# Kernel optimization log

Measured on AMD Instinct MI355X. Metric: run time of the kernel, lower is better.

## Reference

```python
import math
import jax, jax.numpy as jnp
import numpy as np

B, H, W = 2, 128, 128
HW = H * W
D, NH, NL, KS = 256, 8, 1, 5
NP = KS * KS
HD = D // NH
DFF = 1024
KEEP = 0.25
H_SIZE = 188.0
EPS = 1e-5


def _layernorm(x, g, b):
    m = x.mean(-1, keepdims=True)
    v = ((x - m) ** 2).mean(-1, keepdims=True)
    return (x - m) * jax.lax.rsqrt(v + EPS) * g + b


def _mha(q_in, k_in, v_in, w_qkv, b_qkv, w_o, b_o):
    wq, wk, wv = jnp.split(w_qkv, 3, axis=0)
    bq, bk, bv = jnp.split(b_qkv, 3, axis=0)
    def heads(x, w, b):
        y = x @ w.T + b
        return y.reshape(y.shape[0], y.shape[1], NH, HD)
    q, k, v = heads(q_in, wq, bq), heads(k_in, wk, bk), heads(v_in, wv, bv)
    scores = jnp.einsum('bqhd,bkhd->bhqk', q, k) / math.sqrt(HD)
    attn = jax.nn.softmax(scores, axis=-1)
    out = jnp.einsum('bhqk,bkhd->bqhd', attn, v).reshape(q_in.shape[0], q_in.shape[1], D)
    return out @ w_o.T + b_o


def _bilinear(v, grid):
    # v: (B, HW, NH, HD); grid: (B, LQ, NH, NP, 2) normalized (x, y) in [0,1]
    x = grid[..., 0] * W - 0.5
    y = grid[..., 1] * H - 0.5
    x0 = jnp.floor(x); y0 = jnp.floor(y)
    lx = x - x0; ly = y - y0
    x0i = x0.astype(jnp.int32); y0i = y0.astype(jnp.int32)
    bidx = jnp.arange(v.shape[0])[:, None, None, None]
    hidx = jnp.arange(NH)[None, None, :, None]
    def corner(xi, yi, wgt):
        valid = (xi >= 0) & (xi < W) & (yi >= 0) & (yi < H)  # zero-pad outside
        idx = jnp.clip(yi, 0, H - 1) * W + jnp.clip(xi, 0, W - 1)
        s = v[bidx, idx, hidx]  # (B, LQ, NH, NP, HD)
        return s * (wgt * valid)[..., None]
    return (corner(x0i, y0i, (1 - lx) * (1 - ly))
            + corner(x0i + 1, y0i, lx * (1 - ly))
            + corner(x0i, y0i + 1, (1 - lx) * ly)
            + corner(x0i + 1, y0i + 1, lx * ly))


def _where_to_attend(query, ref_windows, lbw, lbb, sow, sob, kernel_indices):
    Bq, L = ref_windows.shape[:2]
    ob = (query @ lbw.T + lbb).reshape(Bq, L, NH, NL, 4)  # with_rotation=False -> 4 vars
    rw = ref_windows[:, :, None, None, :]  # (B, L, 1, 1, 7)
    ref_boxes = rw[..., jnp.array([0, 1, 3, 4])]
    ref_angles = rw[..., 6:7]
    angles = jnp.broadcast_to(ref_angles, (Bq, L, NH, NL, 1))
    boxes = ref_boxes + ob / 8.0 * ref_boxes[..., jnp.array([2, 3, 2, 3])]
    center = boxes[..., None, :2]  # (B, L, NH, NL, 1, 2)
    size = boxes[..., None, 2:]
    cos_a, sin_a = jnp.cos(angles), jnp.sin(angles)
    rot = jnp.stack([cos_a, -sin_a, sin_a, cos_a], -1).reshape(Bq, L, NH, NL, 1, 2, 2)
    dgrid = (query @ sow.T + sob).reshape(Bq, L, NH, NL, NP, 2) / H_SIZE
    fg = kernel_indices * jax.nn.relu(size)              # (B, L, NH, NL, NP, 2)
    fg = center + (fg[..., None, :] * rot).sum(-1)       # rotate then shift
    return fg + dgrid


def _box_attn(query, value, ref_windows, vpw, vpb, law, lab, lbw, lbb, sow, sob, ow, ob_, kernel_indices):
    Bq, LQ = query.shape[:2]
    LV = value.shape[1]
    v = (value @ vpw.T + vpb).reshape(Bq, LV, NH, HD)
    aw = jax.nn.softmax((query @ law.T + lab).reshape(Bq, LQ, NH, NL * NP), axis=-1)
    aw = aw.reshape(Bq, LQ, NH, NL, NP)
    grid = _where_to_attend(query, ref_windows, lbw, lbb, sow, sob, kernel_indices)
    sampled = _bilinear(v, grid[:, :, :, 0])             # single level (NL=1)
    out = (aw[:, :, :, 0, :, None] * sampled).sum(-2).reshape(Bq, LQ, D)
    return out @ ow.T + ob_


def _forward(src, pos, ref_windows, score_mask, in_proj_w, in_proj_b, mha_out_w, mha_out_b,
             value_proj_w, value_proj_b, linear_attn_w, linear_attn_b, linear_box_w, linear_box_b,
             samp_off_w, samp_off_b, ca_out_w, ca_out_b, lin1_w, lin1_b, lin2_w, lin2_b,
             qn_g, qn_b, n1_g, n1_b, n2_g, n2_b, kernel_indices):
    Bq = src.shape[0]
    fg_num = math.ceil(src.shape[1] * KEEP)
    sel_score, indices = jax.lax.top_k(score_mask, fg_num)
    gather = lambda x, i: jnp.take_along_axis(x, i[..., None], axis=1)
    sel_src = gather(src, indices)
    sel_pos = gather(pos, indices)
    sel_ref = gather(ref_windows, indices)
    q_num = math.ceil(fg_num * KEEP)
    q_idx = jax.lax.top_k(sel_score, q_num)[1]
    q_src = gather(sel_src, q_idx)
    q_pos = gather(sel_pos, q_idx)
    qk = q_src + q_pos
    q2 = _mha(qk, qk, q_src, in_proj_w, in_proj_b, mha_out_w, mha_out_b)
    q_src = _layernorm(q_src + q2, qn_g, qn_b)
    brow = jnp.arange(Bq)[:, None]
    sel_src = sel_src.at[brow, q_idx].set(q_src)
    src2 = _box_attn(sel_src + sel_pos, src, sel_ref, value_proj_w, value_proj_b,
                     linear_attn_w, linear_attn_b, linear_box_w, linear_box_b,
                     samp_off_w, samp_off_b, ca_out_w, ca_out_b, kernel_indices)
    sel_src = _layernorm(sel_src + src2, n1_g, n1_b)
    ff = jax.nn.relu(sel_src @ lin1_w.T + lin1_b) @ lin2_w.T + lin2_b
    sel_src = _layernorm(sel_src + ff, n2_g, n2_b)
    return src.at[brow, indices].set(sel_src)


def setup_inputs() -> dict:
    key = jax.random.key(0)
    ks = jax.random.split(key, 16)
    def w(k, shape):
        return jax.random.normal(k, shape, dtype=jnp.float32) * 0.02
    # deformable sampling-offsets bias init (per-head directional grid)
    thetas = np.arange(NH) * (2.0 * np.pi / NH)
    g = np.stack([np.cos(thetas), np.sin(thetas)], -1)
    g = g / np.abs(g).max(-1, keepdims=True)
    g = np.tile(g.reshape(NH, 1, 1, 2), (1, NL, NP, 1)) * (np.arange(NP) + 1).reshape(1, 1, NP, 1)
    samp_off_b = jnp.asarray(g.reshape(-1), dtype=jnp.float32)
    # fixed kernel indices buffer (odd kernel, (x,y) order, /kernel_size)
    ind = np.linspace(-(KS - 1) / 2, (KS - 1) / 2, KS)
    ii, jj = np.meshgrid(ind, ind, indexing='ij')
    kernel_indices = jnp.asarray(np.stack([jj, ii], -1).reshape(-1, 2) / KS, dtype=jnp.float32)
    return dict(
        src=jax.random.normal(ks[0], (B, HW, D), dtype=jnp.float32),
        pos=jax.random.normal(ks[1], (B, HW, D), dtype=jnp.float32),
        src_shape=jnp.array([[H, W]], dtype=jnp.int32),
        src_start_idx=jnp.zeros((1,), dtype=jnp.int32),
        ref_windows=jax.random.uniform(ks[2], (B, HW, 7), dtype=jnp.float32),
        score_mask=jax.random.normal(ks[3], (B, HW), dtype=jnp.float32),
        in_proj_w=w(ks[4], (3 * D, D)), in_proj_b=jnp.zeros((3 * D,), jnp.float32),
        mha_out_w=w(ks[5], (D, D)), mha_out_b=jnp.zeros((D,), jnp.float32),
        value_proj_w=w(ks[6], (D, D)), value_proj_b=jnp.zeros((D,), jnp.float32),
        linear_attn_w=w(ks[7], (NH * NL * NP, D)), linear_attn_b=jnp.zeros((NH * NL * NP,), jnp.float32),
        linear_box_w=w(ks[8], (NL * NH * 4, D)), linear_box_b=jnp.zeros((NL * NH * 4,), jnp.float32),
        samp_off_w=w(ks[9], (NH * NL * NP * 2, D)), samp_off_b=samp_off_b,
        ca_out_w=w(ks[10], (D, D)), ca_out_b=jnp.zeros((D,), jnp.float32),
        lin1_w=w(ks[11], (DFF, D)), lin1_b=jnp.zeros((DFF,), jnp.float32),
        lin2_w=w(ks[12], (D, DFF)), lin2_b=jnp.zeros((D,), jnp.float32),
        qn_g=jnp.ones((D,), jnp.float32), qn_b=jnp.zeros((D,), jnp.float32),
        n1_g=jnp.ones((D,), jnp.float32), n1_b=jnp.zeros((D,), jnp.float32),
        n2_g=jnp.ones((D,), jnp.float32), n2_b=jnp.zeros((D,), jnp.float32),
        kernel_indices=kernel_indices,
    )


def reference(src, pos, src_shape, src_start_idx, ref_windows, score_mask,
              in_proj_w, in_proj_b, mha_out_w, mha_out_b, value_proj_w, value_proj_b,
              linear_attn_w, linear_attn_b, linear_box_w, linear_box_b, samp_off_w, samp_off_b,
              ca_out_w, ca_out_b, lin1_w, lin1_b, lin2_w, lin2_b,
              qn_g, qn_b, n1_g, n1_b, n2_g, n2_b, kernel_indices):
    # src_shape/src_start_idx are static single-level metadata (H, W closed over)
    return _forward(src, pos, ref_windows, score_mask, in_proj_w, in_proj_b, mha_out_w, mha_out_b,
                    value_proj_w, value_proj_b, linear_attn_w, linear_attn_b, linear_box_w, linear_box_b,
                    samp_off_w, samp_off_b, ca_out_w, ca_out_b, lin1_w, lin1_b, lin2_w, lin2_b,
                    qn_g, qn_b, n1_g, n1_b, n2_g, n2_b, kernel_indices)
```

## Files before the change

### kernel.cpp

```cpp
#include <hip/hip_runtime.h>
#include <hip/hip_bf16.h>
#include <math.h>

#define HW_N   16384
#define DIM    256
#define NSEL   4096
#define NQ     1024
#define NHEAD  8
#define HD     32
#define NP_    25
#define DFF_   1024

#define OFF_SELREF  8448LL
#define OFF_SELSRC  65792LL
#define OFF_SELPOS  2162944LL
#define OFF_QUERY   4260096LL
#define OFF_BIG     6357248LL
#define OFF_WBF     10551552LL
#define OFF_F       14745856LL

__device__ __forceinline__ unsigned int f2s(float f) {
    unsigned int u = __float_as_uint(f);
    return (u & 0x80000000u) ? ~u : (u | 0x80000000u);
}

typedef __bf16 bf16x8 __attribute__((ext_vector_type(8)));
typedef __bf16 bf16x4 __attribute__((ext_vector_type(4)));
typedef float  f32x4  __attribute__((ext_vector_type(4)));

extern "C" __global__ __launch_bounds__(256)
void wcvt_kernel(const float* __restrict__ s0, const float* __restrict__ s1,
                 const float* __restrict__ s2, const float* __restrict__ s3,
                 const float* __restrict__ s4, const float* __restrict__ s5,
                 const float* __restrict__ s6, const float* __restrict__ s7,
                 const float* __restrict__ s8, __hip_bfloat16* __restrict__ dst) {
    const long long g = (long long)blockIdx.x * 256 + threadIdx.x;
    const float* s; long long base;
    if      (g < 196608)  { s = s0; base = 0; }
    else if (g < 262144)  { s = s1; base = 196608; }
    else if (g < 327680)  { s = s2; base = 262144; }
    else if (g < 378880)  { s = s3; base = 327680; }
    else if (g < 387072)  { s = s4; base = 378880; }
    else if (g < 489472)  { s = s5; base = 387072; }
    else if (g < 555008)  { s = s6; base = 489472; }
    else if (g < 817152)  { s = s7; base = 555008; }
    else                  { s = s8; base = 817152; }
    dst[g] = __float2bfloat16(s[g - base]);
}

extern "C" __global__ __launch_bounds__(512)
void topk_hist_kernel(const float* __restrict__ score, unsigned int* __restrict__ hist) {
    const int t = threadIdx.x, bx = blockIdx.x, bb = blockIdx.y;
    const int i = bx * 512 + t;
    unsigned int u = f2s(score[(long long)bb * HW_N + i]);
    atomicAdd(&hist[bb * 8192 + (u >> 19)], 1u);
}

extern "C" __global__ __launch_bounds__(1024)
void topk_scan_kernel(const unsigned int* __restrict__ hist, unsigned int* __restrict__ ctrl) {
    __shared__ unsigned int scan[1024];
    const int t = threadIdx.x, bb = blockIdx.x;
    unsigned int loc[8]; unsigned int lsum = 0u;
    #pragma unroll
    for (int k = 0; k < 8; ++k) { loc[k] = hist[bb * 8192 + t * 8 + k]; lsum += loc[k]; }
    scan[t] = lsum;
    __syncthreads();
    for (int off = 1; off < 1024; off <<= 1) {
        unsigned int v = (t + off < 1024) ? scan[t + off] : 0u;
        __syncthreads();
        scan[t] += v;
        __syncthreads();
    }
    unsigned int nxt = (t < 1023) ? scan[t + 1] : 0u;
    unsigned int run = nxt;
    for (int k = 7; k >= 0; --k) {
        run += loc[k];
        unsigned int above = run - loc[k];
        if (run >= 1024u && above < 1024u) { ctrl[bb * 16 + 0] = (unsigned)(t * 8 + k); ctrl[bb * 16 + 1] = 1024u - above; }
        if (run >= 4096u && above < 4096u) { ctrl[bb * 16 + 2] = (unsigned)(t * 8 + k); ctrl[bb * 16 + 3] = 4096u - above; }
    }
}

extern "C" __global__ __launch_bounds__(1024)
void topk_collect_kernel(const float* __restrict__ score, unsigned int* __restrict__ ctrl,
                         unsigned long long* __restrict__ list1,
                         unsigned long long* __restrict__ list2) {
    const int t = threadIdx.x, bx = blockIdx.x, bb = blockIdx.y;
    const int i = bx * 1024 + t;
    const unsigned int T1 = ctrl[bb * 16 + 0], T2 = ctrl[bb * 16 + 2];
    unsigned int u = f2s(score[(long long)bb * HW_N + i]);
    unsigned int bin = u >> 19;
    unsigned long long key = ((unsigned long long)u << 32) | (unsigned int)(~(unsigned int)i);
    if (bin == T1) {
        unsigned int p = atomicAdd(&ctrl[bb * 16 + 4], 1u);
        if (p < 2048u) list1[bb * 2048 + p] = key;
    }
    if (bin == T2 && T2 != T1) {
        unsigned int p = atomicAdd(&ctrl[bb * 16 + 5], 1u);
        if (p < 2048u) list2[bb * 2048 + p] = key;
    }
}

extern "C" __global__ __launch_bounds__(1024)
void topk_classify_kernel(const float* __restrict__ score, unsigned int* __restrict__ ctrl,
                          const unsigned long long* __restrict__ list1,
                          const unsigned long long* __restrict__ list2,
                          int* __restrict__ idx_out) {
    __shared__ unsigned int cA, cB, baseA, baseB;
    const int t = threadIdx.x, bx = blockIdx.x, bb = blockIdx.y;
    const int i = bx * 1024 + t;
    if (t == 0) { cA = 0u; cB = 0u; }
    __syncthreads();
    const unsigned int T1 = ctrl[bb * 16 + 0], need1 = ctrl[bb * 16 + 1];
    const unsigned int T2 = ctrl[bb * 16 + 2], need2 = ctrl[bb * 16 + 3];
    const unsigned int c1 = min(ctrl[bb * 16 + 4], 2048u);
    const unsigned int c2 = min(ctrl[bb * 16 + 5], 2048u);
    unsigned int u = f2s(score[(long long)bb * HW_N + i]);
    unsigned int bin = u >> 19;
    unsigned long long key = ((unsigned long long)u << 32) | (unsigned int)(~(unsigned int)i);
    bool inA = false, inB = false;
    if (bin > T1) {
        inA = true;
    } else if (bin == T1) {
        unsigned int r = 0;
        for (unsigned int q = 0; q < c1; ++q) r += (list1[bb * 2048 + q] > key) ? 1u : 0u;
        if (r < need1) inA = true;
        else if (T2 == T1) inB = (r < need2);
        else inB = true;
    } else if (bin > T2) {
        inB = true;
    } else if (bin == T2) {
        unsigned int r = 0;
        for (unsigned int q = 0; q < c2; ++q) r += (list2[bb * 2048 + q] > key) ? 1u : 0u;
        inB = (r < need2);
    }
    unsigned int sA = 0u, sB = 0u;
    if (inA) sA = atomicAdd(&cA, 1u);
    if (inB) sB = atomicAdd(&cB, 1u);
    __syncthreads();
    if (t == 0) {
        baseA = atomicAdd(&ctrl[bb * 16 + 6], cA);
        baseB = atomicAdd(&ctrl[bb * 16 + 7], cB);
    }
    __syncthreads();
    if (inA) idx_out[bb * NSEL + baseA + sA] = i;
    if (inB) idx_out[bb * NSEL + 1024 + baseB + sB] = i;
}

extern "C" __global__ __launch_bounds__(256)
void gather_kernel(const float* __restrict__ src, const float* __restrict__ pos,
                   const float* __restrict__ refw, const int* __restrict__ idx,
                   float* __restrict__ selsrc, float* __restrict__ selpos,
                   float* __restrict__ selref,
                   __hip_bfloat16* __restrict__ qkb16,
                   __hip_bfloat16* __restrict__ selsrcb) {
    const int s = blockIdx.x, bb = blockIdx.y, t = threadIdx.x;
    const int i = idx[bb * NSEL + s];
    const long long so = ((long long)(bb * NSEL + s)) * DIM;
    const long long go = ((long long)(bb * HW_N + i)) * DIM;
    float sv = src[go + t], pv = pos[go + t];
    selsrc[so + t] = sv;
    selpos[so + t] = pv;
    if (s < NQ) {
        const long long qo = ((long long)(bb * NQ + s)) * DIM + t;
        qkb16[qo] = __float2bfloat16(sv + pv);
        selsrcb[qo] = __float2bfloat16(sv);
    }
    if (t < 7)
        selref[(long long)(bb * NSEL + s) * 7 + t] = refw[(long long)(bb * HW_N + i) * 7 + t];
}

extern "C" __global__ __launch_bounds__(256)
void gemm_kernel(const void* __restrict__ Avp, long long sA,
                 const __hip_bfloat16* __restrict__ W, const float* __restrict__ bias,
                 float* __restrict__ C, long long sC,
                 int M, int N, int K, int relu, int omode, int amode) {
    __shared__ __hip_bfloat16 As[64][72];
    __shared__ __hip_bfloat16 Ws[64][72];
    const int t = threadIdx.x;
    const int n0 = blockIdx.x * 64, m0 = blockIdx.y * 64;
    const long long zoff = (long long)blockIdx.z * sC;
    const int lane = t & 63, wv = t >> 6;
    const int mw = (wv >> 1) * 32, nw = (wv & 1) * 32;
    const int fr = lane & 15;
    const int fk = (lane >> 4) * 8;
    const int sr = t >> 2;
    const int sk = (t & 3) * 16;

    f32x4 acc[2][2];
    #pragma unroll
    for (int i = 0; i < 2; ++i)
        #pragma unroll
        for (int j = 0; j < 2; ++j) acc[i][j] = {0.f, 0.f, 0.f, 0.f};

    const bool wok = (n0 + sr) < N;
    for (int k0 = 0; k0 < K; k0 += 64) {
        uint4 wa = make_uint4(0u, 0u, 0u, 0u), wb = make_uint4(0u, 0u, 0u, 0u);
        if (wok) {
            const __hip_bfloat16* wp = W + (long long)(n0 + sr) * K + k0 + sk;
            wa = *(const uint4*)wp;
            wb = *(const uint4*)(wp + 8);
        }
        if (amode) {
            const __hip_bfloat16* ap = (const __hip_bfloat16*)Avp
                + (long long)blockIdx.z * sA + (long long)(m0 + sr) * K + k0 + sk;
            uint4 aa = *(const uint4*)ap;
            uint4 ab = *(const uint4*)(ap + 8);
            __syncthreads();
            *(uint4*)&As[sr][sk] = aa;
            *(uint4*)&As[sr][sk + 8] = ab;
            *(uint4*)&Ws[sr][sk] = wa;
            *(uint4*)&Ws[sr][sk + 8] = wb;
        } else {
            const float* ap = (const float*)Avp
                + (long long)blockIdx.z * sA + (long long)(m0 + sr) * K + k0 + sk;
            float av[16];
            #pragma unroll
            for (int q = 0; q < 4; ++q) {
                float4 v = *(const float4*)(ap + q * 4);
                av[q * 4 + 0] = v.x; av[q * 4 + 1] = v.y; av[q * 4 + 2] = v.z; av[q * 4 + 3] = v.w;
            }
            __syncthreads();
            #pragma unroll
            for (int q = 0; q < 16; ++q) As[sr][sk + q] = __float2bfloat16(av[q]);
            *(uint4*)&Ws[sr][sk] = wa;
            *(uint4*)&Ws[sr][sk + 8] = wb;
        }
        __syncthreads();
        #pragma unroll
        for (int kk = 0; kk < 64; kk += 32) {
            bf16x8 a0 = *(const bf16x8*)&As[mw + fr][kk + fk];
            bf16x8 a1 = *(const bf16x8*)&As[mw + 16 + fr][kk + fk];
            bf16x8 b0 = *(const bf16x8*)&Ws[nw + fr][kk + fk];
            bf16x8 b1 = *(const bf16x8*)&Ws[nw + 16 + fr][kk + fk];
            acc[0][0] = __builtin_amdgcn_mfma_f32_16x16x32_bf16(a0, b0, acc[0][0], 0, 0, 0);
            acc[0][1] = __builtin_amdgcn_mfma_f32_16x16x32_bf16(a0, b1, acc[0][1], 0, 0, 0);
            acc[1][0] = __builtin_amdgcn_mfma_f32_16x16x32_bf16(a1, b0, acc[1][0], 0, 0, 0);
            acc[1][1] = __builtin_amdgcn_mfma_f32_16x16x32_bf16(a1, b1, acc[1][1], 0, 0, 0);
        }
    }
    const int crow = (lane >> 4) * 4;
    #pragma unroll
    for (int mi = 0; mi < 2; ++mi) {
        #pragma unroll
        for (int ni = 0; ni < 2; ++ni) {
            const int col = n0 + nw + ni * 16 + fr;
            if (col < N) {
                const float bv = bias ? bias[col] : 0.f;
                #pragma unroll
                for (int r = 0; r < 4; ++r) {
                    const int row = m0 + mw + mi * 16 + crow + r;
                    float v = acc[mi][ni][r] + bv;
                    if (relu) v = fmaxf(v, 0.f);
                    if (omode == 0) {
                        C[zoff + (long long)row * N + col] = v;
                    } else if (omode == 1) {
                        ((__hip_bfloat16*)C)[zoff + (long long)row * N + col] = __float2bfloat16(v);
                    } else if (omode == 2) {
                        ((__hip_bfloat16*)C)[zoff + (long long)col * M + row] = __float2bfloat16(v);
                    } else {
                        ((__hip_bfloat16*)C)[zoff + ((long long)(col >> 5) * 16384 + row) * 32 + (col & 31)]
                            = __float2bfloat16(v);
                    }
                }
            }
        }
    }
}

extern "C" __global__ __launch_bounds__(256, 4)
void attn_kernel(const __hip_bfloat16* __restrict__ qkb,
                 const __hip_bfloat16* __restrict__ vT,
                 __hip_bfloat16* __restrict__ attout) {
    __shared__ float sbuf[8256];
    __shared__ float redm[4][16];
    __shared__ float reds[4][16];
    __hip_bfloat16 (*pb)[1032] = (__hip_bfloat16 (*)[1032])sbuf;
    float (*redo)[16][33] = (float (*)[16][33])sbuf;
    const int t = threadIdx.x;
    const int qt = blockIdx.x, h = blockIdx.y, bb = blockIdx.z;
    const int q0 = qt * 16;
    const int lane = t & 63, wv = t >> 6;
    const int fr = lane & 15, g = lane >> 4;
    const int kbase = wv * 256;
    const float scale = 0.17677669529663687f;

    bf16x8 qfrag = *(const bf16x8*)(qkb + ((long long)(bb * NQ + q0 + fr)) * 512 + h * HD + g * 8);

    f32x4 sfr[16];
    #pragma unroll
    for (int half = 0; half < 2; ++half) {
        bf16x8 kf[8];
        #pragma unroll
        for (int j = 0; j < 8; ++j) {
            const int key0 = kbase + (half * 8 + j) * 16;
            kf[j] = *(const bf16x8*)(qkb + ((long long)(bb * NQ + key0 + fr)) * 512 + 256 + h * HD + g * 8);
        }
        __builtin_amdgcn_sched_barrier(0);
        #pragma unroll
        for (int j = 0; j < 8; ++j) {
            f32x4 z = {0.f, 0.f, 0.f, 0.f};
            sfr[half * 8 + j] = __builtin_amdgcn_mfma_f32_16x16x32_bf16(qfrag, kf[j], z, 0, 0, 0);
        }
    }
    #pragma unroll
    for (int kt = 0; kt < 16; ++kt)
        #pragma unroll
        for (int r = 0; r < 4; ++r) sfr[kt][r] *= scale;

    float mxr[4];
    #pragma unroll
    for (int r = 0; r < 4; ++r) {
        float mx = -1e30f;
        #pragma unroll
        for (int kt = 0; kt < 16; ++kt) mx = fmaxf(mx, sfr[kt][r]);
        #pragma unroll
        for (int mm = 1; mm <= 8; mm <<= 1) mx = fmaxf(mx, __shfl_xor(mx, mm, 64));
        float sm = 0.f;
        #pragma unroll
        for (int kt = 0; kt < 16; ++kt) {
            float e = __expf(sfr[kt][r] - mx);
            sfr[kt][r] = e;
            sm += e;
        }
        #pragma unroll
        for (int mm = 1; mm <= 8; mm <<= 1) sm += __shfl_xor(sm, mm, 64);
        mxr[r] = mx;
        if (fr == 0) { redm[wv][4 * g + r] = mx; reds[wv][4 * g + r] = sm; }
    }
    __syncthreads();

    float scl[4];
    #pragma unroll
    for (int r = 0; r < 4; ++r) {
        const int q = 4 * g + r;
        float mm = fmaxf(fmaxf(redm[0][q], redm[1][q]), fmaxf(redm[2][q], redm[3][q]));
        float ll = 0.f;
        #pragma unroll
        for (int w2 = 0; w2 < 4; ++w2) ll += reds[w2][q] * __expf(redm[w2][q] - mm);
        scl[r] = __expf(mxr[r] - mm) / ll;
    }
    #pragma unroll
    for (int kt = 0; kt < 16; ++kt) {
        #pragma unroll
        for (int r = 0; r < 4; ++r) {
            pb[4 * g + r][kbase + kt * 16 + fr] = __float2bfloat16(sfr[kt][r] * scl[r]);
        }
    }

    f32x4 o0 = {0.f, 0.f, 0.f, 0.f}, o1 = {0.f, 0.f, 0.f, 0.f};
    const __hip_bfloat16* vbase = vT + ((long long)bb * DIM + h * HD) * 1024;
    #pragma unroll
    for (int ksb = 0; ksb < 2; ++ksb) {
        bf16x8 pf[4], v0[4], v1[4];
        #pragma unroll
        for (int j = 0; j < 4; ++j) {
            const int key0 = kbase + (ksb * 4 + j) * 32 + g * 8;
            pf[j] = *(const bf16x8*)&pb[fr][key0];
            v0[j] = *(const bf16x8*)(vbase + (long long)fr * 1024 + key0);
            v1[j] = *(const bf16x8*)(vbase + (long long)(16 + fr) * 1024 + key0);
        }
        __builtin_amdgcn_sched_barrier(0);
        #pragma unroll
        for (int j = 0; j < 4; ++j) {
            o0 = __builtin_amdgcn_mfma_f32_16x16x32_bf16(pf[j], v0[j], o0, 0, 0, 0);
            o1 = __builtin_amdgcn_mfma_f32_16x16x32_bf16(pf[j], v1[j], o1, 0, 0, 0);
        }
    }

    __syncthreads();
    #pragma unroll
    for (int r = 0; r < 4; ++r) {
        redo[wv][4 * g + r][fr] = o0[r];
        redo[wv][4 * g + r][16 + fr] = o1[r];
    }
    __syncthreads();
    #pragma unroll
    for (int i = 0; i < 2; ++i) {
        const int idx = t + i * 256;
        const int q = idx >> 5, d = idx & 31;
        float v = redo[0][q][d] + redo[1][q][d] + redo[2][q][d] + redo[3][q][d];
        attout[((long long)(bb * NQ + q0 + q)) * DIM + h * HD + d] = __float2bfloat16(v);
    }
}

extern "C" __global__ __launch_bounds__(256)
void ln_kernel(const float* __restrict__ X, long long sx,
               const float* __restrict__ R, long long sr,
               const float* __restrict__ g, const float* __restrict__ bta,
               float* __restrict__ O, long long so,
               __hip_bfloat16* __restrict__ Ob) {
    __shared__ float red[4];
    const int row = blockIdx.x, bb = blockIdx.y, t = threadIdx.x;
    float x = X[(long long)bb * sx + (long long)row * DIM + t]
            + R[(long long)bb * sr + (long long)row * DIM + t];
    float v = x;
    #pragma unroll
    for (int m = 32; m >= 1; m >>= 1) v += __shfl_xor(v, m, 64);
    if ((t & 63) == 0) red[t >> 6] = v;
    __syncthreads();
    float mean = (red[0] + red[1] + red[2] + red[3]) * (1.f / 256.f);
    __syncthreads();
    float d = x - mean;
    v = d * d;
    #pragma unroll
    for (int m = 32; m >= 1; m >>= 1) v += __shfl_xor(v, m, 64);
    if ((t & 63) == 0) red[t >> 6] = v;
    __syncthreads();
    float var = (red[0] + red[1] + red[2] + red[3]) * (1.f / 256.f);
    float o = d * rsqrtf(var + 1e-5f) * g[t] + bta[t];
    O[(long long)bb * so + (long long)row * DIM + t] = o;
    if (Ob) Ob[(long long)bb * so + (long long)row * DIM + t] = __float2bfloat16(o);
}

extern "C" __global__ __launch_bounds__(256)
void addq_kernel(const float* __restrict__ a, const float* __restrict__ b2,
                 __hip_bfloat16* __restrict__ o) {
    long long i = (long long)blockIdx.x * 256 + threadIdx.x;
    o[i] = __float2bfloat16(a[i] + b2[i]);
}

extern "C" __global__ __launch_bounds__(256)
void boxattn_kernel(const float* __restrict__ aw, const float* __restrict__ ob,
                    const float* __restrict__ dgrid, const float* __restrict__ selref,
                    const __hip_bfloat16* __restrict__ vp, const float* __restrict__ kidx,
                    __hip_bfloat16* __restrict__ boxout) {
    __shared__ float aw_s[400];
    __shared__ float ob_s[64];
    __shared__ float ref_s[112];
    __shared__ float ki_s[50];
    __shared__ float dg_s[800];
    __shared__ float box_s[16][6];
    __shared__ float mx_s[16];
    __shared__ float inv_s[16];
    __shared__ float wq_s[400];
    __shared__ int   i4_s[1600];
    __shared__ float w4_s[1600];
    const int t = threadIdx.x;
    const int combo = blockIdx.x;
    const int bb = combo >> 3, h = combo & 7;
    const int s0 = blockIdx.y * 16;
    const long long base = (long long)bb * NSEL + s0;

    #pragma unroll
    for (int e = t; e < 400; e += 256) {
        const int s = e / 25, p = e - s * 25;
        aw_s[e] = aw[(base + s) * 200 + h * 25 + p];
    }
    if (t < 64)  ob_s[t] = ob[(base + (t >> 2)) * 32 + h * 4 + (t & 3)];
    if (t < 112) ref_s[t] = selref[base * 7 + t];
    if (t < 50)  ki_s[t] = kidx[t];
    #pragma unroll
    for (int e = t; e < 800; e += 256) {
        const int s = e / 50, r = e - s * 50;
        dg_s[e] = dgrid[(base + s) * 400 + h * 50 + r];
    }
    __syncthreads();

    if (t < 16) {
        float mx = -1e30f;
        #pragma unroll
        for (int p = 0; p < NP_; ++p) mx = fmaxf(mx, aw_s[t * NP_ + p]);
        mx_s[t] = mx;
        const float r0 = ref_s[t * 7 + 0], r1 = ref_s[t * 7 + 1];
        const float r3 = ref_s[t * 7 + 3], r4 = ref_s[t * 7 + 4], r6 = ref_s[t * 7 + 6];
        box_s[t][0] = r0 + ob_s[t * 4 + 0] * 0.125f * r3;
        box_s[t][1] = r1 + ob_s[t * 4 + 1] * 0.125f * r4;
        box_s[t][2] = fmaxf(r3 + ob_s[t * 4 + 2] * 0.125f * r3, 0.f);
        box_s[t][3] = fmaxf(r4 + ob_s[t * 4 + 3] * 0.125f * r4, 0.f);
        box_s[t][4] = cosf(r6);
        box_s[t][5] = sinf(r6);
    }
    __syncthreads();

    #pragma unroll
    for (int e = t; e < 400; e += 256) {
        const int s = e / 25, p = e - s * 25;
        const float w = __expf(aw_s[e] - mx_s[s]);
        wq_s[e] = w;
        const float cx = box_s[s][0], cy = box_s[s][1];
        const float sw = box_s[s][2], sh = box_s[s][3];
        const float ca = box_s[s][4], sa = box_s[s][5];
        const float fx = ki_s[p * 2 + 0] * sw;
        const float fy = ki_s[p * 2 + 1] * sh;
        const float gx = cx + ca * fx - sa * fy + dg_s[s * 50 + 2 * p + 0] * (1.f / 188.f);
        const float gy = cy + sa * fx + ca * fy + dg_s[s * 50 + 2 * p + 1] * (1.f / 188.f);
        const float x = gx * 128.f - 0.5f;
        const float y = gy * 128.f - 0.5f;
        const float x0f = floorf(x), y0f = floorf(y);
        const float lx = x - x0f, ly = y - y0f;
        const int x0 = (int)x0f, y0 = (int)y0f;
        #pragma unroll
        for (int c = 0; c < 4; ++c) {
            const int xi = x0 + (c & 1);
            const int yi = y0 + (c >> 1);
            const float wgt = ((c & 1) ? lx : 1.f - lx) * ((c >> 1) ? ly : 1.f - ly);
            const bool valid = (xi >= 0) & (xi < 128) & (yi >= 0) & (yi < 128);
            const int cxi = min(max(xi, 0), 127);
            const int cyi = min(max(yi, 0), 127);
            i4_s[e * 4 + c] = cyi * 128 + cxi;
            w4_s[e * 4 + c] = w * (valid ? wgt : 0.f);
        }
    }
    __syncthreads();

    if (t < 16) {
        float sm = 0.f;
        #pragma unroll
        for (int p = 0; p < NP_; ++p) sm += wq_s[t * NP_ + p];
        inv_s[t] = 1.f / sm;
    }

    {
        const int lane = t & 63;
        const int s_loc = t >> 4;
        const int j2 = (lane >> 2) & 3;
        const int q2 = lane & 3;
        const __hip_bfloat16* vb = vp + ((long long)(bb * 8 + h) * 16384) * 32 + q2 * 8;
        const int ebase = s_loc * 100;
        float a[8] = {0.f, 0.f, 0.f, 0.f, 0.f, 0.f, 0.f, 0.f};
        #pragma unroll
        for (int u = 0; u < 25; ++u) {
            const int ii = ebase + j2 + 4 * u;
            bf16x8 v = *(const bf16x8*)(vb + (long long)i4_s[ii] * 32);
            const float w = w4_s[ii];
            #pragma unroll
            for (int k = 0; k < 8; ++k) a[k] += w * (float)v[k];
        }
        #pragma unroll
        for (int k = 0; k < 8; ++k) a[k] += __shfl_xor(a[k], 4, 64);
        #pragma unroll
        for (int k = 0; k < 8; ++k) a[k] += __shfl_xor(a[k], 8, 64);
        __syncthreads();
        if (j2 == 0) {
            const float inv = inv_s[s_loc];
            __hip_bfloat16* op = boxout + (base + s_loc) * DIM + h * HD + q2 * 8;
            bf16x8 o;
            #pragma unroll
            for (int k = 0; k < 8; ++k) o[k] = __float2bfloat16(a[k] * inv);
            *(bf16x8*)op = o;
        }
    }
}

extern "C" __global__ __launch_bounds__(256)
void scatter_kernel(const int* __restrict__ idx, const float* __restrict__ sel,
                    float* __restrict__ out) {
    const int s = blockIdx.x, bb = blockIdx.y, t = threadIdx.x;
    const int i = idx[bb * NSEL + s];
    out[((long long)(bb * HW_N + i)) * DIM + t] = sel[((long long)(bb * NSEL + s)) * DIM + t];
}

extern "C" void kernel_launch(void* const* d_in, const int* in_sizes, int n_in,
                              void* d_out, int out_size, void* d_ws, size_t ws_size,
                              hipStream_t stream) {
    const float* src          = (const float*)d_in[0];
    const float* pos          = (const float*)d_in[1];
    const float* refw         = (const float*)d_in[4];
    const float* score        = (const float*)d_in[5];
    const float* in_proj_w    = (const float*)d_in[6];
    const float* in_proj_b    = (const float*)d_in[7];
    const float* mha_out_w    = (const float*)d_in[8];
    const float* mha_out_b    = (const float*)d_in[9];
    const float* value_proj_w = (const float*)d_in[10];
    const float* value_proj_b = (const float*)d_in[11];
    const float* lin_attn_w   = (const float*)d_in[12];
    const float* lin_attn_b   = (const float*)d_in[13];
    const float* lin_box_w    = (const float*)d_in[14];
    const float* lin_box_b    = (const float*)d_in[15];
    const float* samp_off_w   = (const float*)d_in[16];
    const float* samp_off_b   = (const float*)d_in[17];
    const float* ca_out_w     = (const float*)d_in[18];
    const float* ca_out_b     = (const float*)d_in[19];
    const float* lin1_w       = (const float*)d_in[20];
    const float* lin1_b       = (const float*)d_in[21];
    const float* lin2_w       = (const float*)d_in[22];
    const float* lin2_b       = (const float*)d_in[23];
    const float* qn_g         = (const float*)d_in[24];
    const float* qn_b         = (const float*)d_in[25];
    const float* n1_g         = (const float*)d_in[26];
    const float* n1_b         = (const float*)d_in[27];
    const float* n2_g         = (const float*)d_in[28];
    const float* n2_b         = (const float*)d_in[29];
    const float* kidx         = (const float*)d_in[30];

    float* w = (float*)d_ws;
    int* idxp = (int*)d_ws;
    float* selref = w + OFF_SELREF;
    float* selsrc = w + OFF_SELSRC;
    float* selpos = w + OFF_SELPOS;
    __hip_bfloat16* boxoutb = (__hip_bfloat16*)(w + OFF_SELPOS);
    __hip_bfloat16* queryb  = (__hip_bfloat16*)(w + OFF_QUERY);
    float* src2   = w + OFF_QUERY;
    __hip_bfloat16* vproj  = (__hip_bfloat16*)(w + OFF_BIG);
    __hip_bfloat16* ffntb  = (__hip_bfloat16*)(w + OFF_BIG);
    __hip_bfloat16* wbf    = (__hip_bfloat16*)(w + OFF_WBF);
    __hip_bfloat16* qkbin   = (__hip_bfloat16*)(w + OFF_F);
    __hip_bfloat16* selsrcb = (__hip_bfloat16*)(w + OFF_F + 262144);
    __hip_bfloat16* qkb = (__hip_bfloat16*)(w + OFF_F + 524288);
    __hip_bfloat16* vT  = (__hip_bfloat16*)(w + OFF_F + 1572864);
    __hip_bfloat16* attoutb = (__hip_bfloat16*)(w + OFF_F + 2097152);
    float* q2     = w + OFF_F + 2621440;
    float* aw     = w + OFF_F;
    float* obuf   = w + OFF_F + 1638400;
    float* dgrid  = w + OFF_F + 1900544;
    float* ff     = w + OFF_F;
    __hip_bfloat16* selsrcb2 = (__hip_bfloat16*)(w + OFF_F + 1048576);
    unsigned int* hist2 = (unsigned int*)(w + OFF_F);
    unsigned int* ctrl2 = hist2 + 16384;
    unsigned long long* list1 = (unsigned long long*)(hist2 + 16448);
    unsigned long long* list2 = list1 + 2 * 2048;
    float* out    = (float*)d_out;

    const long long W_INPROJ = 0, W_MHAOUT = 196608, W_VALUE = 262144,
                    W_LATTN = 327680, W_LBOX = 378880, W_SOFF = 387072,
                    W_CAOUT = 489472, W_LIN1 = 555008, W_LIN2 = 817152;

    hipMemcpyAsync(d_out, src, (size_t)2 * HW_N * DIM * sizeof(float),
                   hipMemcpyDeviceToDevice, stream);

    wcvt_kernel<<<4216, 256, 0, stream>>>(in_proj_w, mha_out_w, value_proj_w,
                                          lin_attn_w, lin_box_w, samp_off_w,
                                          ca_out_w, lin1_w, lin2_w, wbf);

    hipMemsetAsync(hist2, 0, 16448 * sizeof(unsigned int), stream);
    topk_hist_kernel<<<dim3(32, 2), 512, 0, stream>>>(score, hist2);
    topk_scan_kernel<<<2, 1024, 0, stream>>>(hist2, ctrl2);
    topk_collect_kernel<<<dim3(16, 2), 1024, 0, stream>>>(score, ctrl2, list1, list2);
    topk_classify_kernel<<<dim3(16, 2), 1024, 0, stream>>>(score, ctrl2, list1, list2, idxp);

    gather_kernel<<<dim3(NSEL, 2), 256, 0, stream>>>(src, pos, refw, idxp,
                                                     selsrc, selpos, selref,
                                                     qkbin, selsrcb);
    gemm_kernel<<<dim3(8, 16, 2), 256, 0, stream>>>(qkbin, 262144LL, wbf + W_INPROJ, in_proj_b,
                                                    (float*)qkb, 524288LL, NQ, 512, 256, 0, 1, 1);
    gemm_kernel<<<dim3(4, 16, 2), 256, 0, stream>>>(selsrcb, 262144LL, wbf + W_INPROJ + 512 * 256,
                                                    in_proj_b + 512, (float*)vT, 262144LL, NQ, 256, 256, 0, 2, 1);
    attn_kernel<<<dim3(64, 8, 2), 256, 0, stream>>>(qkb, vT, attoutb);
    gemm_kernel<<<dim3(4, 16, 2), 256, 0, stream>>>(attoutb, 262144LL, wbf + W_MHAOUT, mha_out_b,
                                                    q2, 262144LL, NQ, 256, 256, 0, 0, 1);
    ln_kernel<<<dim3(NQ, 2), 256, 0, stream>>>(selsrc, 1048576LL, q2, 262144LL,
                                               qn_g, qn_b, selsrc, 1048576LL, nullptr);
    addq_kernel<<<8192, 256, 0, stream>>>(selsrc, selpos, queryb);
    gemm_kernel<<<dim3(4, 256, 2), 256, 0, stream>>>(src, 4194304LL, wbf + W_VALUE, value_proj_b,
                                                     (float*)vproj, 4194304LL, HW_N, 256, 256, 0, 3, 0);
    gemm_kernel<<<dim3(4, 64, 2), 256, 0, stream>>>(queryb, 1048576LL, wbf + W_LATTN, lin_attn_b,
                                                    aw, 819200LL, NSEL, 200, 256, 0, 0, 1);
    gemm_kernel<<<dim3(1, 64, 2), 256, 0, stream>>>(queryb, 1048576LL, wbf + W_LBOX, lin_box_b,
                                                    obuf, 131072LL, NSEL, 32, 256, 0, 0, 1);
    gemm_kernel<<<dim3(7, 64, 2), 256, 0, stream>>>(queryb, 1048576LL, wbf + W_SOFF, samp_off_b,
                                                    dgrid, 1638400LL, NSEL, 400, 256, 0, 0, 1);
    boxattn_kernel<<<dim3(16, 256), 256, 0, stream>>>(aw, obuf, dgrid, selref, vproj, kidx, boxoutb);
    gemm_kernel<<<dim3(4, 64, 2), 256, 0, stream>>>(boxoutb, 1048576LL, wbf + W_CAOUT, ca_out_b,
                                                    src2, 1048576LL, NSEL, 256, 256, 0, 0, 1);
    ln_kernel<<<dim3(NSEL, 2), 256, 0, stream>>>(selsrc, 1048576LL, src2, 1048576LL,
                                                 n1_g, n1_b, selsrc, 1048576LL, selsrcb2);
    gemm_kernel<<<dim3(16, 64, 2), 256, 0, stream>>>(selsrcb2, 1048576LL, wbf + W_LIN1, lin1_b,
                                                     (float*)ffntb, 4194304LL, NSEL, DFF_, 256, 1, 1, 1);
    gemm_kernel<<<dim3(4, 64, 2), 256, 0, stream>>>(ffntb, 4194304LL, wbf + W_LIN2, lin2_b,
                                                    ff, 1048576LL, NSEL, 256, DFF_, 0, 0, 1);
    ln_kernel<<<dim3(NSEL, 2), 256, 0, stream>>>(selsrc, 1048576LL, ff, 1048576LL,
                                                 n2_g, n2_b, selsrc, 1048576LL, nullptr);
    scatter_kernel<<<dim3(NSEL, 2), 256, 0, stream>>>(idxp, selsrc, out);
}
```

Measured before the change: 404.8 us.

## Add 128x128 LDS-direct GEMM for value projection and FFN, pre-convert src to bf16

Adds a 128x128-tile bf16 MFMA GEMM that fills LDS through global_load_lds 16-byte direct loads, and uses it for the two FFN GEMMs and, when the workspace is large enough, for the value projection. For the value projection, src is first converted to bf16 by a new vectorized kernel so the GEMM reads bf16 instead of converting fp32 on load. The larger tiles raise data reuse per block and cut instruction overhead, but they also mean fewer blocks and an extra conversion pass over src. The new path has no bounds checks and depends on M and N being multiples of 128.

```diff
diff --git a/kernel.cpp b/kernel.cpp
--- a/kernel.cpp
+++ b/kernel.cpp
@@ -18,6 +18,8 @@
 #define OFF_BIG     6357248LL
 #define OFF_WBF     10551552LL
 #define OFF_F       14745856LL
+#define OFF_SRCB    19923200LL
+#define WS_NEED_B   ((OFF_SRCB + 4194304LL) * 4LL)
 
 __device__ __forceinline__ unsigned int f2s(float f) {
     unsigned int u = __float_as_uint(f);
@@ -27,6 +29,12 @@
 typedef __bf16 bf16x8 __attribute__((ext_vector_type(8)));
 typedef __bf16 bf16x4 __attribute__((ext_vector_type(4)));
 typedef float  f32x4  __attribute__((ext_vector_type(4)));
+
+__device__ __forceinline__ void gload16(const void* g, void* l) {
+    __builtin_amdgcn_global_load_lds(
+        (const __attribute__((address_space(1))) void*)g,
+        (__attribute__((address_space(3))) void*)l, 16, 0, 0);
+}
 
 extern "C" __global__ __launch_bounds__(256)
 void wcvt_kernel(const float* __restrict__ s0, const float* __restrict__ s1,
@@ -46,6 +54,19 @@
     else if (g < 817152)  { s = s7; base = 555008; }
     else                  { s = s8; base = 817152; }
     dst[g] = __float2bfloat16(s[g - base]);
+}
+
+extern "C" __global__ __launch_bounds__(256)
+void scvt_kernel(const float* __restrict__ s, __hip_bfloat16* __restrict__ d) {
+    const long long i = ((long long)blockIdx.x * 256 + threadIdx.x) * 8;
+    float4 v0 = *(const float4*)(s + i);
+    float4 v1 = *(const float4*)(s + i + 4);
+    bf16x8 o;
+    o[0] = __float2bfloat16(v0.x); o[1] = __float2bfloat16(v0.y);
+    o[2] = __float2bfloat16(v0.z); o[3] = __float2bfloat16(v0.w);
+    o[4] = __float2bfloat16(v1.x); o[5] = __float2bfloat16(v1.y);
+    o[6] = __float2bfloat16(v1.z); o[7] = __float2bfloat16(v1.w);
+    *(bf16x8*)(d + i) = o;
 }
 
 extern "C" __global__ __launch_bounds__(512)
@@ -262,6 +283,83 @@
                         ((__hip_bfloat16*)C)[zoff + ((long long)(col >> 5) * 16384 + row) * 32 + (col & 31)]
                             = __float2bfloat16(v);
                     }
+                }
+            }
+        }
+    }
+}
+
+extern "C" __global__ __launch_bounds__(256)
+void gemm128_kernel(const __hip_bfloat16* __restrict__ A, long long sA,
+                    const __hip_bfloat16* __restrict__ W, const float* __restrict__ bias,
+                    float* __restrict__ C, long long sC,
+                    int M, int N, int K, int relu, int omode) {
+    __shared__ __hip_bfloat16 As[128][64];
+    __shared__ __hip_bfloat16 Ws[128][64];
+    const int t = threadIdx.x;
+    const int n0 = blockIdx.x * 128, m0 = blockIdx.y * 128;
+    const long long zoffC = (long long)blockIdx.z * sC;
+    const int lane = t & 63, wv = t >> 6;
+    const int mq = (wv >> 1) * 64, nq = (wv & 1) * 64;
+    const int fr = lane & 15;
+    const int fk = (lane >> 4) * 8;
+
+    const __hip_bfloat16* Ab = A + (long long)blockIdx.z * sA;
+
+    f32x4 acc[4][4];
+    #pragma unroll
+    for (int i = 0; i < 4; ++i)
+        #pragma unroll
+        for (int j = 0; j < 4; ++j) acc[i][j] = {0.f, 0.f, 0.f, 0.f};
+
+    const int srow = (lane >> 3);
+    const int scol = (lane & 7) * 8;
+
+    for (int k0 = 0; k0 < K; k0 += 64) {
+        #pragma unroll
+        for (int q = 0; q < 4; ++q) {
+            const int r = (q * 4 + wv) * 8 + srow;
+            gload16(Ab + (long long)(m0 + r) * K + k0 + scol, &As[r][scol]);
+            gload16(W  + (long long)(n0 + r) * K + k0 + scol, &Ws[r][scol]);
+        }
+        __syncthreads();
+        #pragma unroll
+        for (int kk = 0; kk < 64; kk += 32) {
+            bf16x8 av[4], bv[4];
+            #pragma unroll
+            for (int mi = 0; mi < 4; ++mi)
+                av[mi] = *(const bf16x8*)&As[mq + mi * 16 + fr][kk + fk];
+            #pragma unroll
+            for (int ni = 0; ni < 4; ++ni)
+                bv[ni] = *(const bf16x8*)&Ws[nq + ni * 16 + fr][kk + fk];
+            #pragma unroll
+            for (int mi = 0; mi < 4; ++mi)
+                #pragma unroll
+                for (int ni = 0; ni < 4; ++ni)
+                    acc[mi][ni] = __builtin_amdgcn_mfma_f32_16x16x32_bf16(av[mi], bv[ni], acc[mi][ni], 0, 0, 0);
+        }
+        __syncthreads();
+    }
+
+    const int crow = (lane >> 4) * 4;
+    #pragma unroll
+    for (int mi = 0; mi < 4; ++mi) {
+        #pragma unroll
+        for (int ni = 0; ni < 4; ++ni) {
+            const int col = n0 + nq + ni * 16 + fr;
+            const float bvs = bias ? bias[col] : 0.f;
+            #pragma unroll
+            for (int r = 0; r < 4; ++r) {
+                const int row = m0 + mq + mi * 16 + crow + r;
+                float v = acc[mi][ni][r] + bvs;
+                if (relu) v = fmaxf(v, 0.f);
+                if (omode == 0) {
+                    C[zoffC + (long long)row * N + col] = v;
+                } else if (omode == 1) {
+                    ((__hip_bfloat16*)C)[zoffC + (long long)row * N + col] = __float2bfloat16(v);
+                } else {
+                    ((__hip_bfloat16*)C)[zoffC + ((long long)(col >> 5) * 16384 + row) * 32 + (col & 31)]
+                        = __float2bfloat16(v);
                 }
             }
         }
@@ -606,12 +704,15 @@
     float* dgrid  = w + OFF_F + 1900544;
     float* ff     = w + OFF_F;
     __hip_bfloat16* selsrcb2 = (__hip_bfloat16*)(w + OFF_F + 1048576);
+    __hip_bfloat16* srcb = (__hip_bfloat16*)(w + OFF_SRCB);
     unsigned int* hist2 = (unsigned int*)(w + OFF_F);
     unsigned int* ctrl2 = hist2 + 16384;
     unsigned long long* list1 = (unsigned long long*)(hist2 + 16448);
     unsigned long long* list2 = list1 + 2 * 2048;
     float* out    = (float*)d_out;
 
+    const bool big_ws = (ws_size >= (size_t)WS_NEED_B);
+
     const long long W_INPROJ = 0, W_MHAOUT = 196608, W_VALUE = 262144,
                     W_LATTN = 327680, W_LBOX = 378880, W_SOFF = 387072,
                     W_CAOUT = 489472, W_LIN1 = 555008, W_LIN2 = 817152;
@@ -622,6 +723,8 @@
     wcvt_kernel<<<4216, 256, 0, stream>>>(in_proj_w, mha_out_w, value_proj_w,
                                           lin_attn_w, lin_box_w, samp_off_w,
                                           ca_out_w, lin1_w, lin2_w, wbf);
+    if (big_ws)
+        scvt_kernel<<<4096, 256, 0, stream>>>(src, srcb);
 
     hipMemsetAsync(hist2, 0, 16448 * sizeof(unsigned int), stream);
     topk_hist_kernel<<<dim3(32, 2), 512, 0, stream>>>(score, hist2);
@@ -642,8 +745,13 @@
     ln_kernel<<<dim3(NQ, 2), 256, 0, stream>>>(selsrc, 1048576LL, q2, 262144LL,
                                                qn_g, qn_b, selsrc, 1048576LL, nullptr);
     addq_kernel<<<8192, 256, 0, stream>>>(selsrc, selpos, queryb);
-    gemm_kernel<<<dim3(4, 256, 2), 256, 0, stream>>>(src, 4194304LL, wbf + W_VALUE, value_proj_b,
-                                                     (float*)vproj, 4194304LL, HW_N, 256, 256, 0, 3, 0);
+    if (big_ws) {
+        gemm128_kernel<<<dim3(2, 128, 2), 256, 0, stream>>>(srcb, 4194304LL, wbf + W_VALUE, value_proj_b,
+                                                            (float*)vproj, 4194304LL, HW_N, 256, 256, 0, 3);
+    } else {
+        gemm_kernel<<<dim3(4, 256, 2), 256, 0, stream>>>(src, 4194304LL, wbf + W_VALUE, value_proj_b,
+                                                         (float*)vproj, 4194304LL, HW_N, 256, 256, 0, 3, 0);
+    }
     gemm_kernel<<<dim3(4, 64, 2), 256, 0, stream>>>(queryb, 1048576LL, wbf + W_LATTN, lin_attn_b,
                                                     aw, 819200LL, NSEL, 200, 256, 0, 0, 1);
     gemm_kernel<<<dim3(1, 64, 2), 256, 0, stream>>>(queryb, 1048576LL, wbf + W_LBOX, lin_box_b,
@@ -655,10 +763,10 @@
                                                     src2, 1048576LL, NSEL, 256, 256, 0, 0, 1);
     ln_kernel<<<dim3(NSEL, 2), 256, 0, stream>>>(selsrc, 1048576LL, src2, 1048576LL,
                                                  n1_g, n1_b, selsrc, 1048576LL, selsrcb2);
-    gemm_kernel<<<dim3(16, 64, 2), 256, 0, stream>>>(selsrcb2, 1048576LL, wbf + W_LIN1, lin1_b,
-                                                     (float*)ffntb, 4194304LL, NSEL, DFF_, 256, 1, 1, 1);
-    gemm_kernel<<<dim3(4, 64, 2), 256, 0, stream>>>(ffntb, 4194304LL, wbf + W_LIN2, lin2_b,
-                                                    ff, 1048576LL, NSEL, 256, DFF_, 0, 0, 1);
+    gemm128_kernel<<<dim3(8, 32, 2), 256, 0, stream>>>(selsrcb2, 1048576LL, wbf + W_LIN1, lin1_b,
+                                                       (float*)ffntb, 4194304LL, NSEL, DFF_, 256, 1, 1);
+    gemm128_kernel<<<dim3(2, 32, 2), 256, 0, stream>>>(ffntb, 4194304LL, wbf + W_LIN2, lin2_b,
+                                                       ff, 1048576LL, NSEL, 256, DFF_, 0, 0);
     ln_kernel<<<dim3(NSEL, 2), 256, 0, stream>>>(selsrc, 1048576LL, ff, 1048576LL,
                                                  n2_g, n2_b, selsrc, 1048576LL, nullptr);
     scatter_kernel<<<dim3(NSEL, 2), 256, 0, stream>>>(idxp, selsrc, out);
```

Measured after the change: 427.3 us. +5.6%, slower.
